# Optimization experiments

Hardware: AMD Instinct MI355X
Metric: run time of the kernel (lower is better)

## Reference

```python
import jax, jax.numpy as jnp
import numpy as np
import math

B, S, HID = 2, 2048, 2048
NH, NKV, HD = 16, 4, 128
N_REP = NH // NKV
THETA = 1000000.0


def apply_rope(x, position_ids, theta=THETA):
    # x: (B, H, S, D), position_ids: (B, S)
    d = x.shape[-1]
    freqs = 1.0 / (theta ** (jnp.arange(0, d, 2, dtype=jnp.float32) / d))  # (D/2,)
    angles = position_ids.astype(jnp.float32)[:, :, None] * freqs[None, None, :]  # (B,S,D/2)
    cos = jnp.cos(angles)[:, None, :, :]  # (B,1,S,D/2)
    sin = jnp.sin(angles)[:, None, :, :]
    x_even = x[..., 0::2]
    x_odd = x[..., 1::2]
    rot_even = x_even * cos - x_odd * sin
    rot_odd = x_even * sin + x_odd * cos
    out = jnp.stack([rot_even, rot_odd], axis=-1)  # (B,H,S,D/2,2)
    return out.reshape(x.shape)


def setup_inputs() -> dict:
    key = jax.random.key(0)
    ks = jax.random.split(key, 6)
    x = jax.random.normal(ks[0], (B, S, HID), dtype=jnp.float32)
    position_ids = jnp.broadcast_to(jnp.arange(S, dtype=jnp.int64)[None, :], (B, S))
    # causal additive mask: 0 on/below diagonal, large negative above
    causal = jnp.where(jnp.tril(jnp.ones((S, S), dtype=bool)), 0.0, -1e9).astype(jnp.float32)
    attention_mask = jnp.broadcast_to(causal[None, None, :, :], (B, 1, S, S))
    sc = 1.0 / math.sqrt(HID)
    Wq = jax.random.normal(ks[1], (HID, NH * HD), dtype=jnp.float32) * sc
    Wk = jax.random.normal(ks[2], (HID, NKV * HD), dtype=jnp.float32) * sc
    Wv = jax.random.normal(ks[3], (HID, NKV * HD), dtype=jnp.float32) * sc
    Wo = jax.random.normal(ks[4], (NH * HD, HID), dtype=jnp.float32) * sc
    return {"x": x, "position_ids": position_ids, "attention_mask": attention_mask,
            "Wq": Wq, "Wk": Wk, "Wv": Wv, "Wo": Wo}


def reference(x, position_ids, attention_mask, Wq, Wk, Wv, Wo):
    b, s, _ = x.shape
    q = (x @ Wq).reshape(b, s, NH, HD).transpose(0, 2, 1, 3)   # (B,NH,S,D)
    k = (x @ Wk).reshape(b, s, NKV, HD).transpose(0, 2, 1, 3)  # (B,NKV,S,D)
    v = (x @ Wv).reshape(b, s, NKV, HD).transpose(0, 2, 1, 3)
    q = apply_rope(q, position_ids)
    k = apply_rope(k, position_ids)
    # repeat_kv: expand KV heads to match Q heads
    k = jnp.repeat(k, N_REP, axis=1)  # (B,NH,S,D)
    v = jnp.repeat(v, N_REP, axis=1)
    scale = 1.0 / math.sqrt(HD)
    scores = jnp.einsum('bhqd,bhkd->bhqk', q, k) * scale
    scores = scores + attention_mask
    attn = jax.nn.softmax(scores, axis=-1)
    out = jnp.einsum('bhqk,bhkd->bhqd', attn, v)
    out = out.transpose(0, 2, 1, 3).reshape(b, s, NH * HD)
    return out @ Wo
```

## Files before the change

kernel.cpp:

```cpp
#include <hip/hip_runtime.h>
#include <hip/hip_bf16.h>

#define S_LEN 2048
#define HID_D 2048
#define NH 16
#define NKV 4
#define HD 128
#define BATCH 2

typedef __hip_bfloat16 bf16;
using f32x4 = __attribute__((ext_vector_type(4))) float;
using s16x8 = __attribute__((ext_vector_type(8))) short;

struct TrueT { static constexpr bool value = true; };
struct FalseT { static constexpr bool value = false; };

__device__ __forceinline__ f32x4 mfma_16x16x32(s16x8 a, s16x8 b, f32x4 c) {
  return __builtin_amdgcn_mfma_f32_16x16x32_bf16(a, b, c, 0, 0, 0);
}

__device__ __forceinline__ void gload16(const void* g, void* l) {
  __builtin_amdgcn_global_load_lds(
      (const __attribute__((address_space(1))) void*)g,
      (__attribute__((address_space(3))) void*)l, 16, 0, 0);
}

__device__ __forceinline__ unsigned int pk2bf(float a, float b) {
  __hip_bfloat16 lo = __float2bfloat16(a), hi = __float2bfloat16(b);
  return ((unsigned int)*(unsigned short*)&hi << 16) | *(unsigned short*)&lo;
}

__global__ __launch_bounds__(256) void convert_bf16_k(const float* __restrict__ in,
                                                      bf16* __restrict__ out) {
  int i = (blockIdx.x * 256 + threadIdx.x) * 4;
  float4 v = *(const float4*)&in[i];
  out[i + 0] = __float2bfloat16(v.x);
  out[i + 1] = __float2bfloat16(v.y);
  out[i + 2] = __float2bfloat16(v.z);
  out[i + 3] = __float2bfloat16(v.w);
}

__global__ __launch_bounds__(256) void transpose_convert_k(const float* __restrict__ in,
                                                           bf16* __restrict__ out,
                                                           int K, int N) {
  __shared__ float tile[32][33];
  int n0 = blockIdx.x * 32, k0 = blockIdx.y * 32;
  int tx = threadIdx.x, ty = threadIdx.y;
#pragma unroll
  for (int i = ty; i < 32; i += 8) tile[i][tx] = in[(size_t)(k0 + i) * N + n0 + tx];
  __syncthreads();
#pragma unroll
  for (int i = ty; i < 32; i += 8)
    out[(size_t)(n0 + i) * K + k0 + tx] = __float2bfloat16(tile[tx][i]);
}

__global__ __launch_bounds__(512) void gemm256_k(const bf16* __restrict__ A,
                                                 const bf16* __restrict__ Bt,
                                                 bf16* __restrict__ C,
                                                 int M, int N, int K) {
  __shared__ bf16 Asm[2][256 * 64];
  __shared__ bf16 Bsm[2][256 * 64];
  const int tid = threadIdx.x;
  const int lane = tid & 63, wid = tid >> 6;
  const int fr = lane & 15, hi = lane >> 4;

  const int bid = blockIdx.y * gridDim.x + blockIdx.x;
  const int nwg = gridDim.x * gridDim.y;
  const int swz = (bid & 7) * (nwg >> 3) + (bid >> 3);
  const int m0 = (swz % gridDim.x) * 256;
  const int n0 = (swz / gridDim.x) * 256;

  const bf16* Ag = A + (size_t)m0 * K;
  const bf16* Bg = Bt + (size_t)n0 * K;

  auto stageHalf = [&](const bf16* src, bf16* ldsBase, int hr0, int k0) {
#pragma unroll
    for (int c = 0; c < 2; ++c) {
      int byte = tid * 16 + c * 8192;
      int row = byte >> 7;
      int col = byte & 127;
      int colSw = col ^ ((row & 7) << 4);
      gload16((const char*)(src + (size_t)(hr0 + row) * K + k0) + colSw,
              (char*)ldsBase + hr0 * 128 + byte);
    }
  };

  f32x4 acc[4][4][2];
#pragma unroll
  for (int p = 0; p < 4; ++p)
#pragma unroll
    for (int m = 0; m < 4; ++m)
#pragma unroll
      for (int n = 0; n < 2; ++n) acc[p][m][n] = (f32x4){0.f, 0.f, 0.f, 0.f};

  const int NT = K >> 6;
  stageHalf(Ag, &Asm[0][0], 0, 0);
  stageHalf(Bg, &Bsm[0][0], 0, 0);
  stageHalf(Bg, &Bsm[0][0], 128, 0);
  stageHalf(Ag, &Asm[0][0], 128, 0);
  asm volatile("s_waitcnt vmcnt(4)" ::: "memory");
  __builtin_amdgcn_s_barrier();

  for (int t = 0; t < NT; ++t) {
    const int cur = t & 1;
    const int nxt = cur ^ 1;
    const int kn = (t + 1) << 6;
    const bool more = (t + 1) < NT;
#pragma unroll
    for (int p = 0; p < 4; ++p) {
      const int r0 = (p >> 1) * 128 + (wid >> 2) * 64;
      const int c0 = (p & 1) * 128 + (wid & 3) * 32;
      s16x8 af[2][4], bq[2][2];
#pragma unroll
      for (int ks = 0; ks < 2; ++ks) {
#pragma unroll
        for (int m = 0; m < 4; ++m) {
          int r = r0 + m * 16 + fr;
          int cb = (ks * 64 + hi * 16) ^ ((r & 7) << 4);
          af[ks][m] = *(const s16x8*)((const char*)&Asm[cur][0] + r * 128 + cb);
        }
#pragma unroll
        for (int n = 0; n < 2; ++n) {
          int bn = c0 + n * 16 + fr;
          int cb = (ks * 64 + hi * 16) ^ ((bn & 7) << 4);
          bq[ks][n] = *(const s16x8*)((const char*)&Bsm[cur][0] + bn * 128 + cb);
        }
      }
      if (more) {
        if (p == 0) stageHalf(Ag, &Asm[nxt][0], 0, kn);
        else if (p == 1) stageHalf(Bg, &Bsm[nxt][0], 0, kn);
        else if (p == 2) stageHalf(Bg, &Bsm[nxt][0], 128, kn);
        else stageHalf(Ag, &Asm[nxt][0], 128, kn);
        asm volatile("s_waitcnt vmcnt(4)" ::: "memory");
      } else {
        if (p == 0) asm volatile("s_waitcnt vmcnt(2)" ::: "memory");
        else if (p == 1) asm volatile("s_waitcnt vmcnt(0)" ::: "memory");
      }
      __builtin_amdgcn_s_barrier();

      __builtin_amdgcn_s_setprio(1);
#pragma unroll
      for (int m = 0; m < 4; ++m)
#pragma unroll
        for (int n = 0; n < 2; ++n) {
          acc[p][m][n] = mfma_16x16x32(af[0][m], bq[0][n], acc[p][m][n]);
          acc[p][m][n] = mfma_16x16x32(af[1][m], bq[1][n], acc[p][m][n]);
        }
      __builtin_amdgcn_s_setprio(0);
    }
  }

#pragma unroll
  for (int p = 0; p < 4; ++p) {
    const int r0 = (p >> 1) * 128 + (wid >> 2) * 64;
    const int c0 = (p & 1) * 128 + (wid & 3) * 32;
#pragma unroll
    for (int m = 0; m < 4; ++m)
#pragma unroll
      for (int n = 0; n < 2; ++n) {
        const int row = m0 + r0 + m * 16 + hi * 4;
        const int col = n0 + c0 + n * 16 + fr;
#pragma unroll
        for (int r = 0; r < 4; ++r)
          C[(size_t)(row + r) * N + col] = __float2bfloat16(acc[p][m][n][r]);
      }
  }
}

__global__ __launch_bounds__(256) void gemm128sq_k(const bf16* __restrict__ A,
                                                   const bf16* __restrict__ Bt,
                                                   float* __restrict__ C,
                                                   int M, int N, int K) {
  __shared__ bf16 Asm[2][128 * 64];
  __shared__ bf16 Bsm[2][128 * 64];
  const int tid = threadIdx.x;
  const int lane = tid & 63, wid = tid >> 6;
  const int fr = lane & 15, hi = lane >> 4;

  const int bid = blockIdx.y * gridDim.x + blockIdx.x;
  const int nwg = gridDim.x * gridDim.y;
  const int swz = (bid & 7) * (nwg >> 3) + (bid >> 3);
  const int m0 = (swz % gridDim.x) * 128;
  const int n0 = (swz / gridDim.x) * 128;

  const bf16* Ag = A + (size_t)m0 * K;
  const bf16* Bg = Bt + (size_t)n0 * K;

  auto stageT = [&](const bf16* src, bf16* ldsBase, int k0) {
#pragma unroll
    for (int c = 0; c < 4; ++c) {
      int byte = tid * 16 + c * 4096;
      int row = byte >> 7;
      int col = byte & 127;
      int colSw = col ^ ((row & 7) << 4);
      gload16((const char*)(src + (size_t)row * K + k0) + colSw,
              (char*)ldsBase + byte);
    }
  };

  f32x4 acc[4][4];
#pragma unroll
  for (int m = 0; m < 4; ++m)
#pragma unroll
    for (int n = 0; n < 4; ++n) acc[m][n] = (f32x4){0.f, 0.f, 0.f, 0.f};

  const int r0 = (wid >> 1) * 64;
  const int c0 = (wid & 1) * 64;
  const int NT = K >> 6;

  stageT(Ag, &Asm[0][0], 0);
  stageT(Bg, &Bsm[0][0], 0);
  asm volatile("s_waitcnt vmcnt(0)" ::: "memory");
  __builtin_amdgcn_s_barrier();

  for (int t = 0; t < NT; ++t) {
    const int cur = t & 1;
    const int nxt = cur ^ 1;
    const int kn = (t + 1) << 6;
    const bool more = (t + 1) < NT;
#pragma unroll
    for (int p = 0; p < 2; ++p) {
      s16x8 af[4], bq[4];
#pragma unroll
      for (int m = 0; m < 4; ++m) {
        int r = r0 + m * 16 + fr;
        int cb = (p * 64 + hi * 16) ^ ((r & 7) << 4);
        af[m] = *(const s16x8*)((const char*)&Asm[cur][0] + r * 128 + cb);
      }
#pragma unroll
      for (int n = 0; n < 4; ++n) {
        int bn = c0 + n * 16 + fr;
        int cb = (p * 64 + hi * 16) ^ ((bn & 7) << 4);
        bq[n] = *(const s16x8*)((const char*)&Bsm[cur][0] + bn * 128 + cb);
      }
      if (p == 0) {
        if (more) {
          stageT(Ag, &Asm[nxt][0], kn);
          stageT(Bg, &Bsm[nxt][0], kn);
        }
      } else {
        asm volatile("s_waitcnt vmcnt(0)" ::: "memory");
      }
      __builtin_amdgcn_s_barrier();

      __builtin_amdgcn_s_setprio(1);
#pragma unroll
      for (int m = 0; m < 4; ++m)
#pragma unroll
        for (int n = 0; n < 4; ++n)
          acc[m][n] = mfma_16x16x32(af[m], bq[n], acc[m][n]);
      __builtin_amdgcn_s_setprio(0);
    }
  }

#pragma unroll
  for (int m = 0; m < 4; ++m)
#pragma unroll
    for (int n = 0; n < 4; ++n) {
      const int row = m0 + r0 + m * 16 + hi * 4;
      const int col = n0 + c0 + n * 16 + fr;
#pragma unroll
      for (int r = 0; r < 4; ++r)
        C[(size_t)(row + r) * N + col] = acc[m][n][r];
    }
}

__global__ __launch_bounds__(256) void rope_q_k(const bf16* __restrict__ qkv,
                                                const int* __restrict__ pos_ids,
                                                bf16* __restrict__ Q) {
  int idx = blockIdx.x * 256 + threadIdx.x;
  int i = idx & 63;
  int h = (idx >> 6) & 15;
  int s = (idx >> 10) & 2047;
  int b = idx >> 21;
  const float kscale = 0.12751841418861862f;
  float pos = (float)pos_ids[b * S_LEN + s];
  float freq = exp2f((float)i * -0.31143075889569023f);
  float ang = pos * freq;
  float sn, cs;
  sincosf(ang, &sn, &cs);
  const bf16* src = qkv + (size_t)(b * S_LEN + s) * 3072 + h * HD + 2 * i;
  float e = __bfloat162float(src[0]), o = __bfloat162float(src[1]);
  bf16* dst = Q + ((size_t)(b * NH + h) * S_LEN + s) * HD + 2 * i;
  dst[0] = __float2bfloat16((e * cs - o * sn) * kscale);
  dst[1] = __float2bfloat16((e * sn + o * cs) * kscale);
}

__global__ __launch_bounds__(256) void rope_k_k(const bf16* __restrict__ qkv,
                                                const int* __restrict__ pos_ids,
                                                bf16* __restrict__ Kd) {
  int idx = blockIdx.x * 256 + threadIdx.x;
  int i = idx & 63;
  int kvh = (idx >> 6) & 3;
  int s = (idx >> 8) & 2047;
  int b = idx >> 19;
  float pos = (float)pos_ids[b * S_LEN + s];
  float freq = exp2f((float)i * -0.31143075889569023f);
  float ang = pos * freq;
  float sn, cs;
  sincosf(ang, &sn, &cs);
  const bf16* src = qkv + (size_t)(b * S_LEN + s) * 3072 + 2048 + kvh * HD + 2 * i;
  float e = __bfloat162float(src[0]), o = __bfloat162float(src[1]);
  bf16* dst = Kd + ((size_t)(b * NKV + kvh) * S_LEN + s) * HD + 2 * i;
  dst[0] = __float2bfloat16(e * cs - o * sn);
  dst[1] = __float2bfloat16(e * sn + o * cs);
}

__global__ __launch_bounds__(256) void v_trans_k(const bf16* __restrict__ qkv,
                                                 bf16* __restrict__ Vt) {
  __shared__ unsigned short tile[32][33];
  const int tx = threadIdx.x, ty = threadIdx.y;
  const int s0 = blockIdx.x * 32;
  const int d0 = blockIdx.y * 32;
  const int b = blockIdx.z >> 2, kvh = blockIdx.z & 3;
  const unsigned short* src = (const unsigned short*)qkv + 2560 + kvh * HD;
#pragma unroll
  for (int i = ty; i < 32; i += 8)
    tile[i][tx] = src[(size_t)(b * S_LEN + s0 + i) * 3072 + d0 + tx];
  __syncthreads();
  unsigned short* dst = (unsigned short*)Vt + (size_t)(b * NKV + kvh) * HD * S_LEN;
#pragma unroll
  for (int i = ty; i < 32; i += 8)
    dst[(size_t)(d0 + i) * S_LEN + s0 + tx] = tile[tx][i];
}

__global__ __launch_bounds__(256) void attn_k(const bf16* __restrict__ Q,
                                              const bf16* __restrict__ K,
                                              const bf16* __restrict__ Vt,
                                              bf16* __restrict__ Aout) {
  __shared__ bf16 Ks[2][64 * 128];
  __shared__ bf16 Vs[2][128 * 64];
  __shared__ bf16 Ps[4][16 * 64];

  const int lane = threadIdx.x & 63;
  const int wid = threadIdx.x >> 6;
  const int fr = lane & 15;
  const int hi = lane >> 4;
  const int pi = blockIdx.x, h = blockIdx.y, b = blockIdx.z;
  const int kvh = h >> 2;
  const bf16* Qh = Q + (size_t)(b * NH + h) * S_LEN * HD;
  const bf16* Kh = K + (size_t)(b * NKV + kvh) * S_LEN * HD;
  const bf16* Vh = Vt + (size_t)(b * NKV + kvh) * HD * S_LEN;

  const int oB = lane * 16;
  const int rinK = oB >> 8;
  const int rinV = oB >> 7;
  bf16* myP = &Ps[wid][0];
  const int pswz = (fr & 7) << 4;

  auto stageKV = [&](int bufi, int kv0) {
#pragma unroll
    for (int c = 0; c < 4; ++c) {
      int absr = wid * 16 + c * 4 + rinK;
      int colb = (oB & 255) ^ (((absr >> 2) & 7) << 4);
      gload16((const char*)Kh + (size_t)(kv0 + absr) * 256 + colb,
              (char*)&Ks[bufi][0] + (wid * 16 + c * 4) * 256);
    }
#pragma unroll
    for (int c = 0; c < 4; ++c) {
      int absd = wid * 32 + c * 8 + rinV;
      int colb = (oB & 127) ^ ((absd & 7) << 4);
      gload16((const char*)Vh + (size_t)absd * (S_LEN * 2) + (size_t)kv0 * 2 + colb,
              (char*)&Vs[bufi][0] + (wid * 32 + c * 8) * 128);
    }
  };

#pragma unroll 1
  for (int t = 0; t < 2; ++t) {
    const int qb = t ? (31 - pi) : pi;
    const int q0w = qb * 64 + wid * 16;
    const int nsteps = qb + 1;

    s16x8 qf[4];
#pragma unroll
    for (int ks = 0; ks < 4; ++ks)
      qf[ks] = *(const s16x8*)&Qh[(size_t)(q0w + fr) * HD + ks * 32 + hi * 8];

    f32x4 o[8];
#pragma unroll
    for (int ds = 0; ds < 8; ++ds) o[ds] = (f32x4){0.f, 0.f, 0.f, 0.f};
    float lacc[4];
#pragma unroll
    for (int r = 0; r < 4; ++r) lacc[r] = 0.f;

    auto doStep = [&](int kv0, int bufc, auto LASTC) {
      constexpr bool LAST = decltype(LASTC)::value;
      f32x4 sg[4];
#pragma unroll
      for (int kv = 0; kv < 4; ++kv) {
        f32x4 a = (f32x4){0.f, 0.f, 0.f, 0.f};
        const int row = 4 * fr + kv;
#pragma unroll
        for (int ks = 0; ks < 4; ++ks) {
          int cb = (ks * 64 + hi * 16) ^ (((row >> 2) & 7) << 4);
          s16x8 kf = *(const s16x8*)((const char*)&Ks[bufc][0] + row * 256 + cb);
          a = mfma_16x16x32(qf[ks], kf, a);
        }
        sg[kv] = a;
      }

#pragma unroll
      for (int r = 0; r < 4; ++r) {
        float p0 = __builtin_exp2f(sg[0][r]);
        float p1 = __builtin_exp2f(sg[1][r]);
        float p2 = __builtin_exp2f(sg[2][r]);
        float p3 = __builtin_exp2f(sg[3][r]);
        if (LAST) {
          const int qrow = q0w + hi * 4 + r;
          const int kb = kv0 + 4 * fr;
          p0 = (kb <= qrow) ? p0 : 0.f;
          p1 = (kb + 1 <= qrow) ? p1 : 0.f;
          p2 = (kb + 2 <= qrow) ? p2 : 0.f;
          p3 = (kb + 3 <= qrow) ? p3 : 0.f;
        }
        lacc[r] += (p0 + p1) + (p2 + p3);
        const int prow = hi * 4 + r;
        uint2 pv;
        pv.x = pk2bf(p0, p1);
        pv.y = pk2bf(p2, p3);
        *(uint2*)((char*)myP + prow * 128 + ((fr * 8) ^ ((prow & 7) << 4))) = pv;
      }
      __builtin_amdgcn_wave_barrier();

      s16x8 pf[2];
#pragma unroll
      for (int g = 0; g < 2; ++g) {
        int cb = (g * 64 + hi * 16) ^ pswz;
        pf[g] = *(const s16x8*)((const char*)myP + fr * 128 + cb);
      }
      __builtin_amdgcn_wave_barrier();
#pragma unroll
      for (int ds = 0; ds < 8; ++ds) {
#pragma unroll
        for (int g = 0; g < 2; ++g) {
          int d = ds * 16 + fr;
          int cb = (g * 64 + hi * 16) ^ ((d & 7) << 4);
          s16x8 vf = *(const s16x8*)((const char*)&Vs[bufc][0] + d * 128 + cb);
          o[ds] = mfma_16x16x32(pf[g], vf, o[ds]);
        }
      }
    };

    int buf = 0;
    stageKV(0, 0);
    __syncthreads();

    for (int s = 0; s < nsteps - 1; ++s) {
      stageKV(buf ^ 1, s * 64 + 64);
      doStep(s * 64, buf, FalseT{});
      __syncthreads();
      buf ^= 1;
    }
    doStep((nsteps - 1) * 64, buf, TrueT{});
    __syncthreads();

#pragma unroll
    for (int r = 0; r < 4; ++r) {
      float l = lacc[r];
      l += __shfl_xor(l, 1, 16);
      l += __shfl_xor(l, 2, 16);
      l += __shfl_xor(l, 4, 16);
      l += __shfl_xor(l, 8, 16);
      float inv = 1.0f / l;
      const int srow = q0w + hi * 4 + r;
      bf16* orow = Aout + ((size_t)b * S_LEN + srow) * HID_D + h * HD;
#pragma unroll
      for (int ds = 0; ds < 8; ++ds)
        orow[ds * 16 + fr] = __float2bfloat16(o[ds][r] * inv);
    }
  }
}

extern "C" void kernel_launch(void* const* d_in, const int* in_sizes, int n_in,
                              void* d_out, int out_size, void* d_ws, size_t ws_size,
                              hipStream_t stream) {
  const float* x = (const float*)d_in[0];
  const int* pos = (const int*)d_in[1];
  const float* Wq = (const float*)d_in[3];
  const float* Wk = (const float*)d_in[4];
  const float* Wv = (const float*)d_in[5];
  const float* Wo = (const float*)d_in[6];
  float* out = (float*)d_out;

  char* ws = (char*)d_ws;
  size_t off = 0;
  auto alloc = [&](size_t bytes) {
    char* p = ws + off;
    off += (bytes + 255) & ~(size_t)255;
    return p;
  };
  bf16* xb = (bf16*)alloc((size_t)4096 * 2048 * 2);
  bf16* WqkvT = (bf16*)alloc((size_t)3072 * 2048 * 2);
  bf16* WoT = (bf16*)alloc((size_t)2048 * 2048 * 2);
  bf16* qkv = (bf16*)alloc((size_t)4096 * 3072 * 2);
  bf16* Qb = (bf16*)alloc((size_t)BATCH * NH * S_LEN * HD * 2);
  bf16* Kb = (bf16*)alloc((size_t)BATCH * NKV * S_LEN * HD * 2);
  bf16* Vtb = (bf16*)alloc((size_t)BATCH * NKV * HD * S_LEN * 2);
  bf16* aout = (bf16*)qkv;

  convert_bf16_k<<<8192, 256, 0, stream>>>(x, xb);
  dim3 tb(32, 8);
  transpose_convert_k<<<dim3(64, 64), tb, 0, stream>>>(Wq, WqkvT, 2048, 2048);
  transpose_convert_k<<<dim3(16, 64), tb, 0, stream>>>(Wk, WqkvT + (size_t)2048 * 2048, 2048, 512);
  transpose_convert_k<<<dim3(16, 64), tb, 0, stream>>>(Wv, WqkvT + (size_t)2560 * 2048, 2048, 512);
  transpose_convert_k<<<dim3(64, 64), tb, 0, stream>>>(Wo, WoT, 2048, 2048);

  gemm256_k<<<dim3(16, 12), 512, 0, stream>>>(xb, WqkvT, qkv, 4096, 3072, 2048);

  rope_q_k<<<16384, 256, 0, stream>>>(qkv, pos, Qb);
  rope_k_k<<<4096, 256, 0, stream>>>(qkv, pos, Kb);
  v_trans_k<<<dim3(64, 4, 8), tb, 0, stream>>>(qkv, Vtb);

  attn_k<<<dim3(16, NH, BATCH), 256, 0, stream>>>(Qb, Kb, Vtb, aout);

  gemm128sq_k<<<dim3(32, 16), 256, 0, stream>>>(aout, WoT, out, 4096, 2048, 2048);
}
```

Before: 207.3 us.

## Reshape 256x256 GEMM wave tiling to 64x128 per wave with whole-tile staging

The 256x256 bf16 GEMM previously had each wave walk four 64x32 sub-tiles per k-step. It now gives each wave a single 64x128 output tile, swept over two k-halves. Each wave loads 4 A fragments and 8 B fragments per phase, which roughly halves LDS reads per MFMA. The next k-tile's A and B are now staged in one burst at the first phase, with a full vmcnt(0) wait at the second phase. This replaces the earlier staggered half-tile loads, so global-load/compute interleaving is coarser and memory stalls may be less well hidden.

```diff
diff --git a/kernel.cpp b/kernel.cpp
--- a/kernel.cpp
+++ b/kernel.cpp
@@ -73,32 +73,31 @@
   const bf16* Ag = A + (size_t)m0 * K;
   const bf16* Bg = Bt + (size_t)n0 * K;
 
-  auto stageHalf = [&](const bf16* src, bf16* ldsBase, int hr0, int k0) {
-#pragma unroll
-    for (int c = 0; c < 2; ++c) {
+  auto stageT = [&](const bf16* src, bf16* ldsBase, int k0) {
+#pragma unroll
+    for (int c = 0; c < 4; ++c) {
       int byte = tid * 16 + c * 8192;
       int row = byte >> 7;
       int col = byte & 127;
       int colSw = col ^ ((row & 7) << 4);
-      gload16((const char*)(src + (size_t)(hr0 + row) * K + k0) + colSw,
-              (char*)ldsBase + hr0 * 128 + byte);
+      gload16((const char*)(src + (size_t)row * K + k0) + colSw,
+              (char*)ldsBase + byte);
     }
   };
 
-  f32x4 acc[4][4][2];
-#pragma unroll
-  for (int p = 0; p < 4; ++p)
-#pragma unroll
-    for (int m = 0; m < 4; ++m)
-#pragma unroll
-      for (int n = 0; n < 2; ++n) acc[p][m][n] = (f32x4){0.f, 0.f, 0.f, 0.f};
-
+  f32x4 acc[4][8];
+#pragma unroll
+  for (int m = 0; m < 4; ++m)
+#pragma unroll
+    for (int n = 0; n < 8; ++n) acc[m][n] = (f32x4){0.f, 0.f, 0.f, 0.f};
+
+  const int r0 = (wid >> 1) * 64;
+  const int c0 = (wid & 1) * 128;
   const int NT = K >> 6;
-  stageHalf(Ag, &Asm[0][0], 0, 0);
-  stageHalf(Bg, &Bsm[0][0], 0, 0);
-  stageHalf(Bg, &Bsm[0][0], 128, 0);
-  stageHalf(Ag, &Asm[0][0], 128, 0);
-  asm volatile("s_waitcnt vmcnt(4)" ::: "memory");
+
+  stageT(Ag, &Asm[0][0], 0);
+  stageT(Bg, &Bsm[0][0], 0);
+  asm volatile("s_waitcnt vmcnt(0)" ::: "memory");
   __builtin_amdgcn_s_barrier();
 
   for (int t = 0; t < NT; ++t) {
@@ -107,34 +106,27 @@
     const int kn = (t + 1) << 6;
     const bool more = (t + 1) < NT;
 #pragma unroll
-    for (int p = 0; p < 4; ++p) {
-      const int r0 = (p >> 1) * 128 + (wid >> 2) * 64;
-      const int c0 = (p & 1) * 128 + (wid & 3) * 32;
-      s16x8 af[2][4], bq[2][2];
-#pragma unroll
-      for (int ks = 0; ks < 2; ++ks) {
-#pragma unroll
-        for (int m = 0; m < 4; ++m) {
-          int r = r0 + m * 16 + fr;
-          int cb = (ks * 64 + hi * 16) ^ ((r & 7) << 4);
-          af[ks][m] = *(const s16x8*)((const char*)&Asm[cur][0] + r * 128 + cb);
+    for (int p = 0; p < 2; ++p) {
+      s16x8 af[4], bq[8];
+#pragma unroll
+      for (int m = 0; m < 4; ++m) {
+        int r = r0 + m * 16 + fr;
+        int cb = (p * 64 + hi * 16) ^ ((r & 7) << 4);
+        af[m] = *(const s16x8*)((const char*)&Asm[cur][0] + r * 128 + cb);
+      }
+#pragma unroll
+      for (int n = 0; n < 8; ++n) {
+        int bn = c0 + n * 16 + fr;
+        int cb = (p * 64 + hi * 16) ^ ((bn & 7) << 4);
+        bq[n] = *(const s16x8*)((const char*)&Bsm[cur][0] + bn * 128 + cb);
+      }
+      if (p == 0) {
+        if (more) {
+          stageT(Ag, &Asm[nxt][0], kn);
+          stageT(Bg, &Bsm[nxt][0], kn);
         }
-#pragma unroll
-        for (int n = 0; n < 2; ++n) {
-          int bn = c0 + n * 16 + fr;
-          int cb = (ks * 64 + hi * 16) ^ ((bn & 7) << 4);
-          bq[ks][n] = *(const s16x8*)((const char*)&Bsm[cur][0] + bn * 128 + cb);
-        }
-      }
-      if (more) {
-        if (p == 0) stageHalf(Ag, &Asm[nxt][0], 0, kn);
-        else if (p == 1) stageHalf(Bg, &Bsm[nxt][0], 0, kn);
-        else if (p == 2) stageHalf(Bg, &Bsm[nxt][0], 128, kn);
-        else stageHalf(Ag, &Asm[nxt][0], 128, kn);
-        asm volatile("s_waitcnt vmcnt(4)" ::: "memory");
       } else {
-        if (p == 0) asm volatile("s_waitcnt vmcnt(2)" ::: "memory");
-        else if (p == 1) asm volatile("s_waitcnt vmcnt(0)" ::: "memory");
+        asm volatile("s_waitcnt vmcnt(0)" ::: "memory");
       }
       __builtin_amdgcn_s_barrier();
 
@@ -142,29 +134,22 @@
 #pragma unroll
       for (int m = 0; m < 4; ++m)
 #pragma unroll
-        for (int n = 0; n < 2; ++n) {
-          acc[p][m][n] = mfma_16x16x32(af[0][m], bq[0][n], acc[p][m][n]);
-          acc[p][m][n] = mfma_16x16x32(af[1][m], bq[1][n], acc[p][m][n]);
-        }
+        for (int n = 0; n < 8; ++n)
+          acc[m][n] = mfma_16x16x32(af[m], bq[n], acc[m][n]);
       __builtin_amdgcn_s_setprio(0);
     }
   }
 
 #pragma unroll
-  for (int p = 0; p < 4; ++p) {
-    const int r0 = (p >> 1) * 128 + (wid >> 2) * 64;
-    const int c0 = (p & 1) * 128 + (wid & 3) * 32;
-#pragma unroll
-    for (int m = 0; m < 4; ++m)
-#pragma unroll
-      for (int n = 0; n < 2; ++n) {
-        const int row = m0 + r0 + m * 16 + hi * 4;
-        const int col = n0 + c0 + n * 16 + fr;
-#pragma unroll
-        for (int r = 0; r < 4; ++r)
-          C[(size_t)(row + r) * N + col] = __float2bfloat16(acc[p][m][n][r]);
-      }
-  }
+  for (int m = 0; m < 4; ++m)
+#pragma unroll
+    for (int n = 0; n < 8; ++n) {
+      const int row = m0 + r0 + m * 16 + hi * 4;
+      const int col = n0 + c0 + n * 16 + fr;
+#pragma unroll
+      for (int r = 0; r < 4; ++r)
+        C[(size_t)(row + r) * N + col] = __float2bfloat16(acc[m][n][r]);
+    }
 }
 
 __global__ __launch_bounds__(256) void gemm128sq_k(const bf16* __restrict__ A,
```

Measured after the change: 200.5 us (median of 2 runs). 1.03x faster.
